# Kernel tuning notes

Measured on AMD Instinct MI355X. Metric: run time of the kernel, lower is better.

Reference implementation:

```python
import jax, jax.numpy as jnp
import numpy as np

IN_EPS = 1e-3   # torch InstanceNorm2d eps in this module
BN_EPS = 1e-5   # torch BatchNorm2d default eps
KNN_K = 6


def instance_norm(x):
    # x: (B, C, N, 1); normalize per (batch, channel) over spatial dims (affine=False)
    m = jnp.mean(x, axis=(2, 3), keepdims=True)
    v = jnp.var(x, axis=(2, 3), keepdims=True)
    return (x - m) / jnp.sqrt(v + IN_EPS)


def batch_norm(x, gamma, beta):
    # training-mode BatchNorm2d: batch statistics over (B, H, W), biased var
    m = jnp.mean(x, axis=(0, 2, 3), keepdims=True)
    v = jnp.var(x, axis=(0, 2, 3), keepdims=True)
    xn = (x - m) / jnp.sqrt(v + BN_EPS)
    return xn * gamma[None, :, None, None] + beta[None, :, None, None]


def conv1x1(x, w, b):
    # x: (B, Cin, N, K), w: (Cout, Cin), b: (Cout,)
    return jnp.einsum('bcnk,oc->bonk', x, w) + b[None, :, None, None]


def graph_feature(x, k):
    # x: (B, C, P). KNN in feature space + edge feature [x_i, x_i - x_j].
    B, C, P = x.shape
    sq = jnp.sum(x * x, axis=1)                      # (B, P)
    gram = jnp.einsum('bcn,bcm->bnm', x, x)          # (B, P, P)
    pd = 2.0 * gram - sq[:, :, None] - sq[:, None, :]  # negative squared distance
    idx = jax.lax.top_k(pd, k)[1]                    # (B, P, k) nearest (incl. self)
    xt = jnp.transpose(x, (0, 2, 1))                 # (B, P, C)
    neigh = jnp.take_along_axis(xt, idx.reshape(B, P * k)[:, :, None], axis=1)
    neigh = neigh.reshape(B, P, k, C)
    center = jnp.broadcast_to(xt[:, :, None, :], (B, P, k, C))
    edge = jnp.concatenate([center, center - neigh], axis=3)  # (B, P, k, 2C)
    return jnp.transpose(edge, (0, 3, 1, 2))         # (B, 2C, P, k)


def reference(data, dp_gamma, dp_beta, dp_w, dp_b, du_gamma, du_beta, du_w, du_b,
              dg_w1, dg_b1, dg_g1, dg_bb1, dg_w2, dg_b2, dg_g2, dg_bb2, sc_w, sc_b):
    x = data                                         # (B, C=128, N, 1)
    # ---- diff_pool ----
    h = jax.nn.relu(batch_norm(instance_norm(x), dp_gamma, dp_beta))
    embed = conv1x1(h, dp_w, dp_b)                   # (B, K=256, N, 1)
    S = jax.nn.softmax(embed[..., 0], axis=2)        # softmax over points -> (B, K, N)
    x_down = jnp.einsum('bcn,bkn->bck', x[..., 0], S)  # (B, C, K)
    feats = jnp.transpose(x_down, (0, 2, 1))         # transpose(1,2): (B, K, C)
    # ---- DGCNN_MAX_Block: channels=K=256, points=C=128, k=6 ----
    edge = graph_feature(feats, KNN_K)               # (B, 2K, C, k)
    g = jax.nn.relu(batch_norm(conv1x1(edge, dg_w1, dg_b1), dg_g1, dg_bb1))
    g = jax.nn.relu(batch_norm(conv1x1(g, dg_w2, dg_b2), dg_g2, dg_bb2))
    g = jnp.max(g, axis=3)                           # max over neighbors -> (B, K, C)
    x2 = jnp.transpose(g, (0, 2, 1))                 # (B, C, K)
    # ---- diff_unpool ----
    h2 = jax.nn.relu(batch_norm(instance_norm(x), du_gamma, du_beta))
    embed2 = conv1x1(h2, du_w, du_b)                 # (B, K, N, 1)
    S2 = jax.nn.softmax(embed2[..., 0], axis=1)      # softmax over clusters -> (B, K, N)
    x_up = jnp.einsum('bck,bkn->bcn', x2, S2)[..., None]  # (B, C, N, 1)
    out = jnp.concatenate([x, x_up], axis=1)         # (B, 2C, N, 1)
    return conv1x1(out, sc_w, sc_b)                  # (B, C, N, 1)


def setup_inputs() -> dict:
    B, C, N, K = 16, 128, 8192, 256
    ks = jax.random.split(jax.random.key(0), 8)
    s = 0.05
    return {
        'data': jax.random.normal(ks[0], (B, C, N, 1), dtype=jnp.float32),
        'dp_gamma': jnp.ones((C,), jnp.float32), 'dp_beta': jnp.zeros((C,), jnp.float32),
        'dp_w': jax.random.normal(ks[1], (K, C), dtype=jnp.float32) * s,
        'dp_b': jnp.zeros((K,), jnp.float32),
        'du_gamma': jnp.ones((C,), jnp.float32), 'du_beta': jnp.zeros((C,), jnp.float32),
        'du_w': jax.random.normal(ks[2], (K, C), dtype=jnp.float32) * s,
        'du_b': jnp.zeros((K,), jnp.float32),
        'dg_w1': jax.random.normal(ks[3], (K, 2 * K), dtype=jnp.float32) * s,
        'dg_b1': jnp.zeros((K,), jnp.float32),
        'dg_g1': jnp.ones((K,), jnp.float32), 'dg_bb1': jnp.zeros((K,), jnp.float32),
        'dg_w2': jax.random.normal(ks[4], (K, K), dtype=jnp.float32) * s,
        'dg_b2': jnp.zeros((K,), jnp.float32),
        'dg_g2': jnp.ones((K,), jnp.float32), 'dg_bb2': jnp.zeros((K,), jnp.float32),
        'sc_w': jax.random.normal(ks[5], (C, 2 * C), dtype=jnp.float32) * s,
        'sc_b': jnp.zeros((C,), jnp.float32),
    }
```

## Files before the change

### kernel.cpp

```cpp
#include <hip/hip_runtime.h>

typedef __attribute__((ext_vector_type(4))) float f32x4;
typedef __attribute__((ext_vector_type(8))) short s16x8;
typedef __attribute__((ext_vector_type(8))) unsigned short u16x8;
typedef __attribute__((ext_vector_type(4))) unsigned short u16x4;

namespace {
constexpr int B_ = 16, C_ = 128, N_ = 8192, K_ = 256, P_ = 128, NB_ = 6;
constexpr int NSP = 16;
}

__device__ __forceinline__ float bf2f(unsigned short h) {
  return __uint_as_float(((unsigned int)h) << 16);
}
__device__ __forceinline__ unsigned short f2bf(float f) {
  unsigned int u = __float_as_uint(f);
  return (unsigned short)((u + 0x7fffu + ((u >> 16) & 1u)) >> 16);
}
__device__ __forceinline__ void gload_lds16(const void* gsrc, void* ldsdst) {
  __builtin_amdgcn_global_load_lds(
      (const __attribute__((address_space(1))) void*)gsrc,
      (__attribute__((address_space(3))) void*)ldsdst, 16, 0, 0);
}

__global__ __launch_bounds__(256) void k_prep(const float* __restrict__ x,
                                              unsigned short* __restrict__ xh,
                                              unsigned short* __restrict__ xcn,
                                              float* __restrict__ pstS,
                                              float* __restrict__ pstQ) {
  const int chunk = blockIdx.x, b = blockIdx.y;
  const int n0 = chunk * 64;
  __shared__ float ts[64][132];
  __shared__ float rs_[2][128], rq_[2][128];
  const int tid = threadIdx.x;
  for (int i = 0; i < 8; i++) {
    int q = tid + i * 256;
    int n4 = q & 15, c = q >> 4;
    float4 v = *reinterpret_cast<const float4*>(x + (size_t)(b * C_ + c) * N_ + n0 + 4 * n4);
    ts[4 * n4 + 0][c] = v.x; ts[4 * n4 + 1][c] = v.y;
    ts[4 * n4 + 2][c] = v.z; ts[4 * n4 + 3][c] = v.w;
    u16x4 p; p[0] = f2bf(v.x); p[1] = f2bf(v.y); p[2] = f2bf(v.z); p[3] = f2bf(v.w);
    *reinterpret_cast<u16x4*>(xcn + (size_t)(b * C_ + c) * N_ + n0 + 4 * n4) = p;
  }
  __syncthreads();
  for (int i = 0; i < 4; i++) {
    int q = tid + i * 256;
    int cg = q & 15, nn = q >> 4;
    u16x8 o;
#pragma unroll
    for (int j = 0; j < 8; j++) o[j] = f2bf(ts[nn][8 * cg + j]);
    *reinterpret_cast<u16x8*>(xh + (size_t)(b * N_ + n0 + nn) * C_ + 8 * cg) = o;
  }
  {
    int c = tid & 127, h = tid >> 7;
    float s = 0.f, ss = 0.f;
    for (int nn = h * 32; nn < h * 32 + 32; nn++) { float v = ts[nn][c]; s += v; ss += v * v; }
    rs_[h][c] = s; rq_[h][c] = ss;
  }
  __syncthreads();
  if (tid < 128) {
    pstS[(chunk * 16 + b) * 128 + tid] = rs_[0][tid] + rs_[1][tid];
    pstQ[(chunk * 16 + b) * 128 + tid] = rq_[0][tid] + rq_[1][tid];
  }
}

__global__ __launch_bounds__(256) void k_wconv(const float* __restrict__ dpw,
                                               const float* __restrict__ duw,
                                               const float* __restrict__ scw,
                                               const float* __restrict__ w1,
                                               const float* __restrict__ w2,
                                               unsigned short* __restrict__ dpwh,
                                               unsigned short* __restrict__ duwh,
                                               unsigned short* __restrict__ scah,
                                               unsigned short* __restrict__ scbh,
                                               unsigned short* __restrict__ w1sh,
                                               unsigned short* __restrict__ w1bh,
                                               unsigned short* __restrict__ w2h) {
  int t = blockIdx.x * 256 + threadIdx.x;
  if (t < 65536) {
    int o = t >> 8, k = t & 255;
    float vb = w1[(size_t)o * 512 + 256 + k];
    w1sh[t] = f2bf(w1[(size_t)o * 512 + k] + vb);
    w1bh[t] = f2bf(vb);
    w2h[t] = f2bf(w2[t]);
  }
  if (t < 32768) { dpwh[t] = f2bf(dpw[t]); duwh[t] = f2bf(duw[t]); }
  if (t < 16384) {
    int o = t >> 7, c = t & 127;
    scah[t] = f2bf(scw[o * 256 + c]);
    scbh[t] = f2bf(scw[o * 256 + 128 + c]);
  }
}

__global__ __launch_bounds__(256) void k_instat_fin(const float* __restrict__ pstS,
                                                    const float* __restrict__ pstQ,
                                                    float* __restrict__ m_o,
                                                    float* __restrict__ v_o,
                                                    float* __restrict__ r_o) {
  int e = blockIdx.x * 256 + threadIdx.x;
  int b = e >> 7, c = e & 127;
  float s = 0.f, q = 0.f;
  for (int ch = 0; ch < 128; ch++) {
    s += pstS[(ch * 16 + b) * 128 + c];
    q += pstQ[(ch * 16 + b) * 128 + c];
  }
  float m = s / N_;
  float v = q / N_ - m * m;
  m_o[e] = m; v_o[e] = v; r_o[e] = rsqrtf(v + 1e-3f);
}

__global__ void k_affine(const float* __restrict__ m_in, const float* __restrict__ v_in,
                         const float* __restrict__ r_in,
                         const float* __restrict__ dpg, const float* __restrict__ dpb,
                         const float* __restrict__ dug, const float* __restrict__ dub,
                         float* __restrict__ a_dp, float* __restrict__ d_dp,
                         float* __restrict__ a_du, float* __restrict__ d_du) {
  int c = threadIdx.x;
  float V = 0.f;
  for (int b = 0; b < B_; b++) { float v = v_in[b * C_ + c]; V += v / (v + 1e-3f); }
  V *= (1.f / B_);
  float R = rsqrtf(V + 1e-5f);
  float gdp = dpg[c], bdp = dpb[c], gdu = dug[c], bdu = dub[c];
  for (int b = 0; b < B_; b++) {
    int i = b * C_ + c;
    float r = r_in[i], m = m_in[i];
    float sdp = r * R * gdp;
    a_dp[i] = sdp; d_dp[i] = -m * sdp + bdp;
    float sdu = r * R * gdu;
    a_du[i] = sdu; d_du[i] = -m * sdu + bdu;
  }
}

__global__ __launch_bounds__(512) void k_dp_fused(const unsigned short* __restrict__ xh,
                                                  const unsigned short* __restrict__ xcn,
                                                  const unsigned short* __restrict__ dpwh,
                                                  const float* __restrict__ a_dp,
                                                  const float* __restrict__ d_dp,
                                                  const float* __restrict__ dpbias,
                                                  float* __restrict__ part,
                                                  float* __restrict__ pS) {
  const int sp = blockIdx.x, b = blockIdx.y;
  const int nbase = sp * (N_ / NSP);
  __shared__ __align__(16) unsigned short bufW[256 * 128];
  __shared__ __align__(16) unsigned short bufH[64 * 128];
  __shared__ __align__(16) unsigned short bufP[256 * 64];
  __shared__ __align__(16) unsigned short bufC[128 * 64];
  __shared__ float bias_s[256], aff_as[128], aff_ds[128];
  const int tid = threadIdx.x, lane = tid & 63, wid = tid >> 6;
  const int wr = wid >> 1, wc = wid & 1, l15 = lane & 15, l4 = lane >> 4;
  if (tid < 256) bias_s[tid] = dpbias[tid];
  if (tid < 128) { aff_as[tid] = a_dp[b * C_ + tid]; aff_ds[tid] = d_dp[b * C_ + tid]; }
#pragma unroll
  for (int i = 0; i < 8; i++) {
    int call = wid * 8 + i;
    int row = call * 4 + (lane >> 4);
    int gch = (lane & 15) ^ (row & 7);
    gload_lds16(dpwh + (size_t)row * C_ + gch * 8, bufW + call * 512);
  }
#pragma unroll
  for (int i = 0; i < 2; i++) {
    int call = wid * 2 + i;
    int row = call * 4 + (lane >> 4);
    int gch = (lane & 15) ^ (row & 7);
    gload_lds16(xh + (size_t)(b * N_ + nbase + row) * C_ + gch * 8, bufH + call * 512);
  }
#pragma unroll
  for (int i = 0; i < 2; i++) {
    int call = wid * 2 + i;
    int row = call * 8 + (lane >> 3);
    int gch = (lane & 7) ^ (row & 7);
    gload_lds16(xcn + (size_t)(b * C_ + row) * N_ + nbase + gch * 8, bufC + call * 512);
  }
  __syncthreads();
#pragma unroll
  for (int i = 0; i < 2; i++) {
    int q = tid + i * 512;
    int row = q >> 4, p = q & 15;
    int cb = (p ^ (row & 7)) * 8;
    u16x8 v = *reinterpret_cast<const u16x8*>(bufH + q * 8);
    u16x8 h;
#pragma unroll
    for (int j = 0; j < 8; j++)
      h[j] = f2bf(fmaxf(fmaf(aff_as[cb + j], bf2f(v[j]), aff_ds[cb + j]), 0.f));
    *reinterpret_cast<u16x8*>(bufH + q * 8) = h;
  }
  __syncthreads();
  s16x8 onesf;
#pragma unroll
  for (int j = 0; j < 8; j++) onesf[j] = (short)0x3F80;
  f32x4 acc2[2][8] = {};
  f32x4 accS[8] = {};
  for (int nc = 0; nc < N_ / NSP; nc += 64) {
    const int n0n = nbase + nc + 64;
    const bool more = (nc + 64) < (N_ / NSP);
    f32x4 acc1[4][2] = {};
#pragma unroll
    for (int ks = 0; ks < 128; ks += 32) {
      const int ch = (ks >> 3) + l4;
      s16x8 af[4], bh[2];
#pragma unroll
      for (int m = 0; m < 4; m++) {
        int row = wr * 64 + m * 16 + l15;
        af[m] = *reinterpret_cast<const s16x8*>(bufW + row * 128 + ((ch ^ (row & 7)) << 3));
      }
#pragma unroll
      for (int nq = 0; nq < 2; nq++) {
        int row = wc * 32 + nq * 16 + l15;
        bh[nq] = *reinterpret_cast<const s16x8*>(bufH + row * 128 + ((ch ^ (row & 7)) << 3));
      }
#pragma unroll
      for (int m = 0; m < 4; m++)
#pragma unroll
        for (int nq = 0; nq < 2; nq++)
          acc1[m][nq] = __builtin_amdgcn_mfma_f32_16x16x32_bf16(af[m], bh[nq], acc1[m][nq], 0, 0, 0);
    }
#pragma unroll
    for (int m = 0; m < 4; m++)
#pragma unroll
      for (int nq = 0; nq < 2; nq++) {
        int kl = wr * 64 + m * 16 + 4 * l4;
        int nl = wc * 32 + nq * 16 + l15;
#pragma unroll
        for (int r = 0; r < 4; r++) {
          unsigned short v = f2bf(__expf(acc1[m][nq][r] + bias_s[kl + r]));
          bufP[(kl + r) * 64 + ((((nl >> 3) ^ ((kl + r) & 7)) << 3) | (nl & 7))] = v;
        }
      }
    __syncthreads();
    if (more) {
#pragma unroll
      for (int i = 0; i < 2; i++) {
        int call = wid * 2 + i;
        int row = call * 4 + (lane >> 4);
        int gch = (lane & 15) ^ (row & 7);
        gload_lds16(xh + (size_t)(b * N_ + n0n + row) * C_ + gch * 8, bufH + call * 512);
      }
    }
#pragma unroll
    for (int ks = 0; ks < 64; ks += 32) {
      const int ch = (ks >> 3) + l4;
      s16x8 af2[2], bp[8];
#pragma unroll
      for (int m = 0; m < 2; m++) {
        int row = wr * 32 + m * 16 + l15;
        af2[m] = *reinterpret_cast<const s16x8*>(bufC + row * 64 + ((ch ^ (row & 7)) << 3));
      }
#pragma unroll
      for (int nn = 0; nn < 8; nn++) {
        int row = wc * 128 + nn * 16 + l15;
        bp[nn] = *reinterpret_cast<const s16x8*>(bufP + row * 64 + ((ch ^ (row & 7)) << 3));
      }
#pragma unroll
      for (int m = 0; m < 2; m++)
#pragma unroll
        for (int nn = 0; nn < 8; nn++)
          acc2[m][nn] = __builtin_amdgcn_mfma_f32_16x16x32_bf16(af2[m], bp[nn], acc2[m][nn], 0, 0, 0);
      if (wr == 0) {
#pragma unroll
        for (int nn = 0; nn < 8; nn++)
          accS[nn] = __builtin_amdgcn_mfma_f32_16x16x32_bf16(onesf, bp[nn], accS[nn], 0, 0, 0);
      }
    }
    __syncthreads();
    if (more) {
#pragma unroll
      for (int i = 0; i < 2; i++) {
        int q = tid + i * 512;
        int row = q >> 4, p = q & 15;
        int cb = (p ^ (row & 7)) * 8;
        u16x8 v = *reinterpret_cast<const u16x8*>(bufH + q * 8);
        u16x8 h;
#pragma unroll
        for (int j = 0; j < 8; j++)
          h[j] = f2bf(fmaxf(fmaf(aff_as[cb + j], bf2f(v[j]), aff_ds[cb + j]), 0.f));
        *reinterpret_cast<u16x8*>(bufH + q * 8) = h;
      }
#pragma unroll
      for (int i = 0; i < 2; i++) {
        int call = wid * 2 + i;
        int row = call * 8 + (lane >> 3);
        int gch = (lane & 7) ^ (row & 7);
        gload_lds16(xcn + (size_t)(b * C_ + row) * N_ + n0n + gch * 8, bufC + call * 512);
      }
      __syncthreads();
    }
  }
#pragma unroll
  for (int m = 0; m < 2; m++)
#pragma unroll
    for (int nn = 0; nn < 8; nn++) {
      int c = wr * 32 + m * 16 + 4 * l4;
      int k = wc * 128 + nn * 16 + l15;
#pragma unroll
      for (int r = 0; r < 4; r++)
        part[((size_t)(sp * B_ + b) * C_ + c + r) * K_ + k] = acc2[m][nn][r];
    }
  if (wr == 0 && l4 == 0) {
#pragma unroll
    for (int nn = 0; nn < 8; nn++)
      pS[((size_t)sp * 16 + b) * 256 + wc * 128 + nn * 16 + l15] = accS[nn][0];
  }
}

__global__ __launch_bounds__(256) void k_rowfin(const float* __restrict__ pS,
                                                float* __restrict__ rden) {
  int e = blockIdx.x * 256 + threadIdx.x;
  int b = e >> 8, k = e & 255;
  float s = 0.f;
  for (int sp = 0; sp < NSP; sp++) s += pS[((size_t)sp * 16 + b) * 256 + k];
  rden[e] = 1.f / s;
}

__global__ __launch_bounds__(256) void k_xdown_red(const float* __restrict__ part,
                                                   const float* __restrict__ rden,
                                                   float* __restrict__ xd,
                                                   unsigned short* __restrict__ xdh) {
  int e = blockIdx.x * 256 + threadIdx.x;
  int k = e % K_;
  int b = e / (K_ * C_);
  float s = 0.f;
  for (int sp = 0; sp < NSP; sp++) s += part[(size_t)sp * (B_ * C_ * K_) + e];
  float v = s * rden[b * K_ + k];
  xd[e] = v;
  xdh[e] = f2bf(v);
}

__global__ __launch_bounds__(256) void k_knn(const float* __restrict__ xd,
                                             int* __restrict__ idx) {
  const int p0 = blockIdx.x * 8, b = blockIdx.y;
  __shared__ float A[8][256];
  __shared__ float Bt[32][132];
  __shared__ float pd_s[8][129];
  __shared__ float sq_s[128], sqh[128];
  const int tid = threadIdx.x;
#pragma unroll
  for (int i = 0; i < 2; i++) {
    int t = tid + i * 256;
    int pp = t >> 6, k4 = t & 63;
    float4 v = *reinterpret_cast<const float4*>(xd + (size_t)(b * C_ + p0 + pp) * K_ + 4 * k4);
    *reinterpret_cast<float4*>(&A[pp][4 * k4]) = v;
  }
  const int q = tid & 127, h = tid >> 7;
  float acc[4] = {};
  float sqacc = 0.f;
  for (int k0 = 0; k0 < K_; k0 += 32) {
    for (int i = 0; i < 4; i++) {
      int t = tid + i * 256;
      int qq = t >> 3, k4 = t & 7;
      float4 v = *reinterpret_cast<const float4*>(xd + (size_t)(b * C_ + qq) * K_ + k0 + 4 * k4);
      Bt[4 * k4 + 0][qq] = v.x; Bt[4 * k4 + 1][qq] = v.y;
      Bt[4 * k4 + 2][qq] = v.z; Bt[4 * k4 + 3][qq] = v.w;
    }
    __syncthreads();
    for (int kk = 0; kk < 32; ++kk) {
      float bv = Bt[kk][q];
#pragma unroll
      for (int i = 0; i < 4; ++i) acc[i] = fmaf(A[h * 4 + i][k0 + kk], bv, acc[i]);
    }
    {
      float s = 0.f;
      for (int kk = h * 16; kk < h * 16 + 16; kk++) { float v = Bt[kk][q]; s += v * v; }
      sqacc += s;
    }
    __syncthreads();
  }
  if (h == 1) sqh[q] = sqacc;
#pragma unroll
  for (int i = 0; i < 4; ++i) pd_s[h * 4 + i][q] = acc[i];
  __syncthreads();
  if (tid < 128) sq_s[tid] = sqacc + sqh[tid];
  __syncthreads();
  const int wv = tid >> 6, lane = tid & 63;
  for (int r = 0; r < 2; r++) {
    int p = wv * 2 + r;
    float v0 = 2.f * pd_s[p][lane] - sq_s[lane];
    float v1 = 2.f * pd_s[p][lane + 64] - sq_s[lane + 64];
    int q0 = lane, q1 = lane + 64;
#pragma unroll
    for (int j = 0; j < NB_; j++) {
      float bv; int bq;
      if (v0 > v1 || (v0 == v1 && q0 < q1)) { bv = v0; bq = q0; } else { bv = v1; bq = q1; }
#pragma unroll
      for (int o = 32; o > 0; o >>= 1) {
        float ov = __shfl_xor(bv, o); int oq = __shfl_xor(bq, o);
        if (ov > bv || (ov == bv && oq < bq)) { bv = ov; bq = oq; }
      }
      if (lane == 0) idx[(b * P_ + p0 + p) * NB_ + j] = bq;
      if (q0 == bq) v0 = -3.0e38f;
      if (q1 == bq) v1 = -3.0e38f;
    }
  }
}

__global__ __launch_bounds__(256) void k_uv_mfma(const unsigned short* __restrict__ xdh,
                                                 const unsigned short* __restrict__ w1sh,
                                                 const unsigned short* __restrict__ w1bh,
                                                 float* __restrict__ Ut, float* __restrict__ Vt) {
  const int o0 = blockIdx.x * 128, which = blockIdx.y, b = blockIdx.z;
  __shared__ __align__(16) unsigned char smemraw[128 * 132 * 4];
  unsigned short* tA = (unsigned short*)smemraw;
  unsigned short* tB = tA + 128 * 128;
  const unsigned short* wsel = which ? w1bh : w1sh;
  const int tid = threadIdx.x, lane = tid & 63, wid = tid >> 6;
  const int wr = wid >> 1, wc = wid & 1, l15 = lane & 15, l4 = lane >> 4;
  f32x4 acc[4][4] = {};
  for (int kh = 0; kh < 256; kh += 128) {
#pragma unroll
    for (int i = 0; i < 8; i++) {
      int call = wid * 8 + i;
      int row = call * 4 + (lane >> 4);
      int gch = (lane & 15) ^ (row & 7);
      gload_lds16(wsel + (size_t)(o0 + row) * 256 + kh + gch * 8, tA + call * 512);
      gload_lds16(xdh + (size_t)(b * P_ + row) * 256 + kh + gch * 8, tB + call * 512);
    }
    __syncthreads();
#pragma unroll
    for (int ks = 0; ks < 128; ks += 32) {
      const int ch = (ks >> 3) + l4;
      s16x8 af[4], bfv[4];
#pragma unroll
      for (int m = 0; m < 4; m++) {
        int row = wr * 64 + m * 16 + l15;
        af[m] = *reinterpret_cast<const s16x8*>(tA + row * 128 + ((ch ^ (row & 7)) << 3));
      }
#pragma unroll
      for (int n = 0; n < 4; n++) {
        int row = wc * 64 + n * 16 + l15;
        bfv[n] = *reinterpret_cast<const s16x8*>(tB + row * 128 + ((ch ^ (row & 7)) << 3));
      }
#pragma unroll
      for (int m = 0; m < 4; m++)
#pragma unroll
        for (int n = 0; n < 4; n++)
          acc[m][n] = __builtin_amdgcn_mfma_f32_16x16x32_bf16(af[m], bfv[n], acc[m][n], 0, 0, 0);
    }
    __syncthreads();
  }
  float (*ef)[132] = (float(*)[132])smemraw;
#pragma unroll
  for (int m = 0; m < 4; m++)
#pragma unroll
    for (int n = 0; n < 4; n++) {
      int ol = wr * 64 + m * 16 + 4 * l4;
      int pl = wc * 64 + n * 16 + l15;
#pragma unroll
      for (int r = 0; r < 4; r++) ef[pl][ol + r] = acc[m][n][r];
    }
  __syncthreads();
  float* outp = which ? Vt : Ut;
  for (int i = 0; i < 16; i++) {
    int q = tid + i * 256;
    int pl = q >> 5, c4 = q & 31;
    float4 v = *reinterpret_cast<const float4*>(&ef[pl][c4 * 4]);
    *reinterpret_cast<float4*>(outp + (size_t)(b * P_ + pl) * 256 + o0 + c4 * 4) = v;
  }
}

__global__ __launch_bounds__(256) void k_edge_t(const float* __restrict__ Ut,
                                                const float* __restrict__ Vt,
                                                const int* __restrict__ idx,
                                                const float* __restrict__ b1,
                                                unsigned short* __restrict__ g1h) {
  __shared__ float b1s[256];
  const int tid = threadIdx.x;
  b1s[tid] = b1[tid];
  __syncthreads();
  const int row0 = blockIdx.x * 16;
  for (int r = 0; r < 16; r++) {
    int row = row0 + r;
    int b = row / 768, pj = row % 768, p = pj / 6;
    int q = idx[(b * P_ + p) * NB_ + (pj % 6)];
    float v = Ut[(size_t)(b * P_ + p) * 256 + tid] + b1s[tid]
            - Vt[(size_t)(b * P_ + q) * 256 + tid];
    g1h[(size_t)row * 256 + tid] = f2bf(v);
  }
}

__global__ __launch_bounds__(256) void k_bnstat_t(const unsigned short* __restrict__ gt,
                                                  float* __restrict__ partS,
                                                  float* __restrict__ partQ) {
  const int tid = threadIdx.x;
  const size_t row0 = (size_t)blockIdx.x * 256;
  float s = 0.f, ss = 0.f;
  for (int r = 0; r < 256; r++) {
    float v = bf2f(gt[(row0 + r) * 256 + tid]);
    s += v; ss += v * v;
  }
  partS[blockIdx.x * 256 + tid] = s;
  partQ[blockIdx.x * 256 + tid] = ss;
}

__global__ __launch_bounds__(256) void k_conv2_mfma(const unsigned short* __restrict__ g1h,
                                                    const unsigned short* __restrict__ w2h,
                                                    const float* __restrict__ b2,
                                                    const float* __restrict__ partS,
                                                    const float* __restrict__ partQ,
                                                    const float* __restrict__ gamma,
                                                    const float* __restrict__ beta,
                                                    unsigned short* __restrict__ g2h) {
  const int n0 = blockIdx.x * 128, o0 = blockIdx.y * 128, b = blockIdx.z;
  __shared__ __align__(16) unsigned short smem[2 * 128 * 128];
  unsigned short* tA = smem;
  unsigned short* tB = smem + 128 * 128;
  __shared__ float scs[256], shs[256], b2s[128];
  const int tid = threadIdx.x, lane = tid & 63, wid = tid >> 6;
  const int wr = wid >> 1, wc = wid & 1, l15 = lane & 15, l4 = lane >> 4;
  {
    float s = 0.f, q = 0.f;
    for (int i = 0; i < 48; i++) { s += partS[i * 256 + tid]; q += partQ[i * 256 + tid]; }
    const float cnt = (float)(B_ * P_ * NB_);
    float m = s / cnt, var = q / cnt - m * m;
    float scale = gamma[tid] * rsqrtf(var + 1e-5f);
    scs[tid] = scale; shs[tid] = -m * scale + beta[tid];
  }
  if (tid < 128) b2s[tid] = b2[o0 + tid];
  f32x4 acc[4][4] = {};
  for (int kh = 0; kh < 256; kh += 128) {
#pragma unroll
    for (int i = 0; i < 8; i++) {
      int call = wid * 8 + i;
      int row = call * 4 + (lane >> 4);
      int gch = (lane & 15) ^ (row & 7);
      gload_lds16(w2h + (size_t)(o0 + row) * 256 + kh + gch * 8, tA + call * 512);
      gload_lds16(g1h + (size_t)(b * 768 + n0 + row) * 256 + kh + gch * 8, tB + call * 512);
    }
    __syncthreads();
#pragma unroll
    for (int ks = 0; ks < 128; ks += 32) {
      const int ch = (ks >> 3) + l4;
      s16x8 af[4], bfv[4];
#pragma unroll
      for (int m = 0; m < 4; m++) {
        int row = wr * 64 + m * 16 + l15;
        af[m] = *reinterpret_cast<const s16x8*>(tA + row * 128 + ((ch ^ (row & 7)) << 3));
      }
#pragma unroll
      for (int n = 0; n < 4; n++) {
        int row = wc * 64 + n * 16 + l15;
        s16x8 raw = *reinterpret_cast<const s16x8*>(tB + row * 128 + ((ch ^ (row & 7)) << 3));
        s16x8 h;
#pragma unroll
        for (int j = 0; j < 8; j++) {
          int c = kh + ks + 8 * l4 + j;
          h[j] = (short)f2bf(fmaxf(fmaf(scs[c], bf2f((unsigned short)raw[j]), shs[c]), 0.f));
        }
        bfv[n] = h;
      }
#pragma unroll
      for (int m = 0; m < 4; m++)
#pragma unroll
        for (int n = 0; n < 4; n++)
          acc[m][n] = __builtin_amdgcn_mfma_f32_16x16x32_bf16(af[m], bfv[n], acc[m][n], 0, 0, 0);
    }
    __syncthreads();
  }
  unsigned short (*e_s)[136] = reinterpret_cast<unsigned short(*)[136]>(smem);
#pragma unroll
  for (int m = 0; m < 4; m++)
#pragma unroll
    for (int n = 0; n < 4; n++) {
      int ol = wr * 64 + m * 16 + 4 * l4;
      int nl = wc * 64 + n * 16 + l15;
#pragma unroll
      for (int r = 0; r < 4; r++)
        e_s[nl][ol + r] = f2bf(acc[m][n][r] + b2s[ol + r]);
    }
  __syncthreads();
  for (int i = 0; i < 8; i++) {
    int q = tid + i * 256;
    int og = q & 15, nl = q >> 4;
    u16x8 v = *reinterpret_cast<const u16x8*>(&e_s[nl][8 * og]);
    *reinterpret_cast<u16x8*>(g2h + (size_t)(b * 768 + n0 + nl) * 256 + o0 + 8 * og) = v;
  }
}

__global__ __launch_bounds__(256) void k_gmax_t(const unsigned short* __restrict__ g2h,
                                                const float* __restrict__ partS,
                                                const float* __restrict__ partQ,
                                                const float* __restrict__ gamma,
                                                const float* __restrict__ beta,
                                                unsigned short* __restrict__ gmaxh) {
  const int o0 = blockIdx.x * 128, b = blockIdx.y;
  __shared__ float scS[128], shS[128];
  const int tid = threadIdx.x;
  if (tid < 128) {
    int o = o0 + tid;
    float s = 0.f, q = 0.f;
    for (int i = 0; i < 48; i++) { s += partS[i * 256 + o]; q += partQ[i * 256 + o]; }
    const float cnt = (float)(B_ * P_ * NB_);
    float m = s / cnt, var = q / cnt - m * m;
    float scale = gamma[o] * rsqrtf(var + 1e-5f);
    scS[tid] = scale; shS[tid] = -m * scale + beta[o];
  }
  __syncthreads();
  const int ol = tid & 127, ph = tid >> 7;
  const int o = o0 + ol;
  const float sc = scS[ol], sh = shS[ol];
  for (int p8 = ph * 64; p8 < ph * 64 + 64; p8 += 8) {
    u16x8 pack;
#pragma unroll
    for (int pi = 0; pi < 8; pi++) {
      int p = p8 + pi;
      float m = 0.f;
#pragma unroll
      for (int j = 0; j < NB_; j++) {
        float v = bf2f(g2h[(size_t)(b * 768 + p * 6 + j) * 256 + o]);
        m = fmaxf(m, fmaf(sc, v, sh));
      }
      pack[pi] = f2bf(m);
    }
    *reinterpret_cast<u16x8*>(gmaxh + (size_t)(b * 256 + o) * P_ + p8) = pack;
  }
}

__global__ __launch_bounds__(256) void k_m2_mfma(const unsigned short* __restrict__ gmaxh,
                                                 const unsigned short* __restrict__ scbh,
                                                 unsigned short* __restrict__ M2h) {
  const int k0 = blockIdx.x * 128, b = blockIdx.y;
  __shared__ __align__(16) unsigned short smem[2 * 128 * 128];
  unsigned short* tA = smem;
  unsigned short* tB = smem + 128 * 128;
  const int tid = threadIdx.x, lane = tid & 63, wid = tid >> 6;
  const int wr = wid >> 1, wc = wid & 1, l15 = lane & 15, l4 = lane >> 4;
#pragma unroll
  for (int i = 0; i < 8; i++) {
    int call = wid * 8 + i;
    int row = call * 4 + (lane >> 4);
    int gch = (lane & 15) ^ (row & 7);
    gload_lds16(scbh + (size_t)row * P_ + gch * 8, tA + call * 512);
    gload_lds16(gmaxh + (size_t)(b * 256 + k0 + row) * P_ + gch * 8, tB + call * 512);
  }
  __syncthreads();
  f32x4 acc[4][4] = {};
#pragma unroll
  for (int ks = 0; ks < 128; ks += 32) {
    const int ch = (ks >> 3) + l4;
    s16x8 af[4], bfv[4];
#pragma unroll
    for (int m = 0; m < 4; m++) {
      int row = wr * 64 + m * 16 + l15;
      af[m] = *reinterpret_cast<const s16x8*>(tA + row * 128 + ((ch ^ (row & 7)) << 3));
    }
#pragma unroll
    for (int n = 0; n < 4; n++) {
      int row = wc * 64 + n * 16 + l15;
      bfv[n] = *reinterpret_cast<const s16x8*>(tB + row * 128 + ((ch ^ (row & 7)) << 3));
    }
#pragma unroll
    for (int m = 0; m < 4; m++)
#pragma unroll
      for (int n = 0; n < 4; n++)
        acc[m][n] = __builtin_amdgcn_mfma_f32_16x16x32_bf16(af[m], bfv[n], acc[m][n], 0, 0, 0);
  }
  __syncthreads();
  unsigned short (*e_s)[136] = reinterpret_cast<unsigned short(*)[136]>(smem);
#pragma unroll
  for (int m = 0; m < 4; m++)
#pragma unroll
    for (int n = 0; n < 4; n++) {
      int ol = wr * 64 + m * 16 + 4 * l4;
      int kl = wc * 64 + n * 16 + l15;
#pragma unroll
      for (int r = 0; r < 4; r++)
        e_s[ol + r][kl] = f2bf(acc[m][n][r]);
    }
  __syncthreads();
  for (int i = 0; i < 8; i++) {
    int q = tid + i * 256;
    int kg = q & 15, oo = q >> 4;
    u16x8 v = *reinterpret_cast<const u16x8*>(&e_s[oo][8 * kg]);
    *reinterpret_cast<u16x8*>(M2h + (size_t)(b * C_ + oo) * K_ + k0 + 8 * kg) = v;
  }
}

__global__ __launch_bounds__(512) void k_final_f(const unsigned short* __restrict__ xh,
                                                 const unsigned short* __restrict__ duwh,
                                                 const float* __restrict__ dubias,
                                                 const float* __restrict__ a_du,
                                                 const float* __restrict__ d_du,
                                                 const unsigned short* __restrict__ M2h,
                                                 const unsigned short* __restrict__ scah,
                                                 const float* __restrict__ scb,
                                                 float* __restrict__ out) {
  const int n0 = blockIdx.x * 64, b = blockIdx.y;
  __shared__ __align__(16) unsigned short bufX[64 * 128];
  __shared__ __align__(16) unsigned short bufA[128 * 128];
  __shared__ __align__(16) unsigned short bufP[64 * 128];
  __shared__ float aff_as[128], aff_ds[128], scb_s[128], bias_s[128];
  __shared__ float psum_s[64], psum2[4][64];
  const int tid = threadIdx.x, lane = tid & 63, wid = tid >> 6;
  const int wr = wid >> 1, wc = wid & 1, l15 = lane & 15, l4 = lane >> 4;
  if (tid < 128) {
    aff_as[tid] = a_du[b * C_ + tid];
    aff_ds[tid] = d_du[b * C_ + tid];
    scb_s[tid] = scb[tid];
  }
  if (tid < 64) psum_s[tid] = 0.f;
#pragma unroll
  for (int i = 0; i < 2; i++) {
    int call = wid * 2 + i;
    int row = call * 4 + (lane >> 4);
    int gch = (lane & 15) ^ (row & 7);
    gload_lds16(xh + (size_t)(b * N_ + n0 + row) * C_ + gch * 8, bufX + call * 512);
  }
#pragma unroll
  for (int i = 0; i < 4; i++) {
    int call = wid * 4 + i;
    int row = call * 4 + (lane >> 4);
    int gch = (lane & 15) ^ (row & 7);
    gload_lds16(scah + (size_t)row * C_ + gch * 8, bufA + call * 512);
  }
  __syncthreads();
  f32x4 accA[2][2] = {};
#pragma unroll
  for (int ks = 0; ks < 128; ks += 32) {
    const int ch = (ks >> 3) + l4;
    s16x8 af[2], bh[2];
#pragma unroll
    for (int m = 0; m < 2; m++) {
      int row = wr * 32 + m * 16 + l15;
      af[m] = *reinterpret_cast<const s16x8*>(bufA + row * 128 + ((ch ^ (row & 7)) << 3));
    }
#pragma unroll
    for (int nq = 0; nq < 2; nq++) {
      int row = wc * 32 + nq * 16 + l15;
      bh[nq] = *reinterpret_cast<const s16x8*>(bufX + row * 128 + ((ch ^ (row & 7)) << 3));
    }
#pragma unroll
    for (int m = 0; m < 2; m++)
#pragma unroll
      for (int nq = 0; nq < 2; nq++)
        accA[m][nq] = __builtin_amdgcn_mfma_f32_16x16x32_bf16(af[m], bh[nq], accA[m][nq], 0, 0, 0);
  }
  __syncthreads();
#pragma unroll
  for (int i = 0; i < 2; i++) {
    int q = tid + i * 512;
    int row = q >> 4, p = q & 15;
    int cb = (p ^ (row & 7)) * 8;
    u16x8 v = *reinterpret_cast<const u16x8*>(bufX + q * 8);
    u16x8 h;
#pragma unroll
    for (int j = 0; j < 8; j++)
      h[j] = f2bf(fmaxf(fmaf(aff_as[cb + j], bf2f(v[j]), aff_ds[cb + j]), 0.f));
    *reinterpret_cast<u16x8*>(bufX + q * 8) = h;
  }
  f32x4 acc[2][2] = {};
  for (int kh = 0; kh < K_; kh += 128) {
    if (tid < 128) bias_s[tid] = dubias[kh + tid];
#pragma unroll
    for (int i = 0; i < 4; i++) {
      int call = wid * 4 + i;
      int row = call * 4 + (lane >> 4);
      int gch = (lane & 15) ^ (row & 7);
      gload_lds16(duwh + (size_t)(kh + row) * C_ + gch * 8, bufA + call * 512);
    }
    __syncthreads();
    f32x4 acc1[2][2] = {};
#pragma unroll
    for (int ks = 0; ks < 128; ks += 32) {
      const int ch = (ks >> 3) + l4;
      s16x8 af[2], bh[2];
#pragma unroll
      for (int m = 0; m < 2; m++) {
        int row = wr * 32 + m * 16 + l15;
        af[m] = *reinterpret_cast<const s16x8*>(bufA + row * 128 + ((ch ^ (row & 7)) << 3));
      }
#pragma unroll
      for (int nq = 0; nq < 2; nq++) {
        int row = wc * 32 + nq * 16 + l15;
        bh[nq] = *reinterpret_cast<const s16x8*>(bufX + row * 128 + ((ch ^ (row & 7)) << 3));
      }
#pragma unroll
      for (int m = 0; m < 2; m++)
#pragma unroll
        for (int nq = 0; nq < 2; nq++)
          acc1[m][nq] = __builtin_amdgcn_mfma_f32_16x16x32_bf16(af[m], bh[nq], acc1[m][nq], 0, 0, 0);
    }
    __syncthreads();
#pragma unroll
    for (int i = 0; i < 4; i++) {
      int call = wid * 4 + i;
      int row = call * 4 + (lane >> 4);
      int gch = (lane & 15) ^ (row & 7);
      gload_lds16(M2h + (size_t)(b * C_ + row) * K_ + kh + gch * 8, bufA + call * 512);
    }
    float pn[2] = {0.f, 0.f};
#pragma unroll
    for (int m = 0; m < 2; m++)
#pragma unroll
      for (int nq = 0; nq < 2; nq++) {
        int kl = wr * 32 + m * 16 + 4 * l4;
        int nl = wc * 32 + nq * 16 + l15;
        u16x4 pk;
#pragma unroll
        for (int r = 0; r < 4; r++) {
          unsigned short v = f2bf(__expf(acc1[m][nq][r] + bias_s[kl + r]));
          pk[r] = v;
          pn[nq] += bf2f(v);
        }
        int swzbase = (((kl >> 3) ^ (nl & 7)) << 3) | (kl & 7);
        *reinterpret_cast<u16x4*>(bufP + nl * 128 + swzbase) = pk;
      }
#pragma unroll
    for (int nq = 0; nq < 2; nq++) {
      pn[nq] += __shfl_xor(pn[nq], 16);
      pn[nq] += __shfl_xor(pn[nq], 32);
      if (l4 == 0) psum2[wr][wc * 32 + nq * 16 + l15] = pn[nq];
    }
    __syncthreads();
    if (tid < 64)
      psum_s[tid] += psum2[0][tid] + psum2[1][tid] + psum2[2][tid] + psum2[3][tid];
#pragma unroll
    for (int ks = 0; ks < 128; ks += 32) {
      const int ch = (ks >> 3) + l4;
      s16x8 af[2], bh[2];
#pragma unroll
      for (int m = 0; m < 2; m++) {
        int row = wr * 32 + m * 16 + l15;
        af[m] = *reinterpret_cast<const s16x8*>(bufA + row * 128 + ((ch ^ (row & 7)) << 3));
      }
#pragma unroll
      for (int nq = 0; nq < 2; nq++) {
        int row = wc * 32 + nq * 16 + l15;
        bh[nq] = *reinterpret_cast<const s16x8*>(bufP + row * 128 + ((ch ^ (row & 7)) << 3));
      }
#pragma unroll
      for (int m = 0; m < 2; m++)
#pragma unroll
        for (int nq = 0; nq < 2; nq++)
          acc[m][nq] = __builtin_amdgcn_mfma_f32_16x16x32_bf16(af[m], bh[nq], acc[m][nq], 0, 0, 0);
    }
    __syncthreads();
  }
#pragma unroll
  for (int m = 0; m < 2; m++)
#pragma unroll
    for (int nq = 0; nq < 2; nq++) {
      float rv = 1.f / psum_s[wc * 32 + nq * 16 + l15];
      int o = wr * 32 + m * 16 + 4 * l4;
      int nn = n0 + wc * 32 + nq * 16 + l15;
#pragma unroll
      for (int r = 0; r < 4; r++)
        out[(size_t)(b * C_ + o + r) * N_ + nn] =
            acc[m][nq][r] * rv + accA[m][nq][r] + scb_s[o + r];
    }
}

extern "C" void kernel_launch(void* const* d_in, const int* in_sizes, int n_in,
                              void* d_out, int out_size, void* d_ws, size_t ws_size,
                              hipStream_t stream) {
  (void)in_sizes; (void)n_in; (void)out_size; (void)ws_size;
  const float* x      = (const float*)d_in[0];
  const float* dpg    = (const float*)d_in[1];
  const float* dpb    = (const float*)d_in[2];
  const float* dpw    = (const float*)d_in[3];
  const float* dpbias = (const float*)d_in[4];
  const float* dug    = (const float*)d_in[5];
  const float* dub    = (const float*)d_in[6];
  const float* duw    = (const float*)d_in[7];
  const float* dubias = (const float*)d_in[8];
  const float* w1     = (const float*)d_in[9];
  const float* b1     = (const float*)d_in[10];
  const float* g1g    = (const float*)d_in[11];
  const float* g1b    = (const float*)d_in[12];
  const float* w2     = (const float*)d_in[13];
  const float* b2     = (const float*)d_in[14];
  const float* g2g    = (const float*)d_in[15];
  const float* g2b    = (const float*)d_in[16];
  const float* scw    = (const float*)d_in[17];
  const float* scb    = (const float*)d_in[18];
  float* out = (float*)d_out;
  float* ws  = (float*)d_ws;

  float* part = ws;
  unsigned short* g1h   = (unsigned short*)ws;
  unsigned short* g2h   = g1h + 3145728;
  unsigned short* gmaxh = g2h + 3145728;
  unsigned short* xh  = (unsigned short*)(ws + 16777216);
  unsigned short* xcn = (unsigned short*)(ws + 25165824);
  float* base  = ws + 33554432;
  float* m_in  = base;
  float* v_in  = m_in + 2048;
  float* r_in  = v_in + 2048;
  float* a_dp  = r_in + 2048;
  float* d_dp  = a_dp + 2048;
  float* a_du  = d_dp + 2048;
  float* d_du  = a_du + 2048;
  float* rden  = d_du + 2048;
  float* xd    = rden + 4096;
  float* Ut    = xd + 524288;
  float* Vt    = Ut + 524288;
  int*   idxb  = (int*)(Vt + 524288);
  float* partS = (float*)(idxb + 12288);
  float* partQ = partS + 12288;
  float* pstS  = partQ + 12288;
  float* pstQ  = pstS + 262144;
  float* pS    = pstQ + 262144;
  unsigned short* xdh  = (unsigned short*)(pS + 65536);
  unsigned short* dpwh = xdh + 524288;
  unsigned short* duwh = dpwh + 32768;
  unsigned short* scah = duwh + 32768;
  unsigned short* scbh = scah + 16384;
  unsigned short* w1sh = scbh + 16384;
  unsigned short* w1bh = w1sh + 65536;
  unsigned short* w2h  = w1bh + 65536;
  unsigned short* M2h  = w2h + 65536;

  k_prep<<<dim3(128, 16), 256, 0, stream>>>(x, xh, xcn, pstS, pstQ);
  k_wconv<<<dim3(256), 256, 0, stream>>>(dpw, duw, scw, w1, w2,
                                         dpwh, duwh, scah, scbh, w1sh, w1bh, w2h);
  k_instat_fin<<<dim3(8), 256, 0, stream>>>(pstS, pstQ, m_in, v_in, r_in);
  k_affine<<<1, 128, 0, stream>>>(m_in, v_in, r_in, dpg, dpb, dug, dub, a_dp, d_dp, a_du, d_du);
  k_dp_fused<<<dim3(NSP, 16), 512, 0, stream>>>(xh, xcn, dpwh, a_dp, d_dp, dpbias, part, pS);
  k_rowfin<<<dim3(16), 256, 0, stream>>>(pS, rden);
  k_xdown_red<<<dim3(2048), 256, 0, stream>>>(part, rden, xd, xdh);
  k_knn<<<dim3(16, 16), 256, 0, stream>>>(xd, idxb);
  k_uv_mfma<<<dim3(2, 2, 16), 256, 0, stream>>>(xdh, w1sh, w1bh, Ut, Vt);
  k_edge_t<<<dim3(768), 256, 0, stream>>>(Ut, Vt, idxb, b1, g1h);
  k_bnstat_t<<<dim3(48), 256, 0, stream>>>(g1h, partS, partQ);
  k_conv2_mfma<<<dim3(6, 2, 16), 256, 0, stream>>>(g1h, w2h, b2, partS, partQ, g1g, g1b, g2h);
  k_bnstat_t<<<dim3(48), 256, 0, stream>>>(g2h, partS, partQ);
  k_gmax_t<<<dim3(2, 16), 256, 0, stream>>>(g2h, partS, partQ, g2g, g2b, gmaxh);
  k_m2_mfma<<<dim3(2, 16), 256, 0, stream>>>(gmaxh, scbh, M2h);
  k_final_f<<<dim3(128, 16), 512, 0, stream>>>(xh, duwh, dubias, a_du, d_du, M2h, scah, scb, out);
}
```

Baseline: 208.3 us.

## Derive channel-major x tile in LDS instead of writing and reloading xcn

Stops k_prep from writing a second channel-major bf16 copy of the input (xcn) and stops k_dp_fused from loading it. The fused kernel now loads the point-major xh tile into a new raw buffer and transposes it into bufC with scalar LDS stores while applying the affine+ReLU. This removes a full global write and read of the bf16 input, at the cost of an extra LDS buffer (more shared memory per block) and many scattered 2-byte LDS writes that may cause bank conflicts.

After: 214.4 us. 2.9% more time.

```diff
diff --git a/kernel.cpp b/kernel.cpp
--- a/kernel.cpp
+++ b/kernel.cpp
@@ -25,7 +25,6 @@
 
 __global__ __launch_bounds__(256) void k_prep(const float* __restrict__ x,
                                               unsigned short* __restrict__ xh,
-                                              unsigned short* __restrict__ xcn,
                                               float* __restrict__ pstS,
                                               float* __restrict__ pstQ) {
   const int chunk = blockIdx.x, b = blockIdx.y;
@@ -39,8 +38,6 @@
     float4 v = *reinterpret_cast<const float4*>(x + (size_t)(b * C_ + c) * N_ + n0 + 4 * n4);
     ts[4 * n4 + 0][c] = v.x; ts[4 * n4 + 1][c] = v.y;
     ts[4 * n4 + 2][c] = v.z; ts[4 * n4 + 3][c] = v.w;
-    u16x4 p; p[0] = f2bf(v.x); p[1] = f2bf(v.y); p[2] = f2bf(v.z); p[3] = f2bf(v.w);
-    *reinterpret_cast<u16x4*>(xcn + (size_t)(b * C_ + c) * N_ + n0 + 4 * n4) = p;
   }
   __syncthreads();
   for (int i = 0; i < 4; i++) {
@@ -132,7 +129,6 @@
 }
 
 __global__ __launch_bounds__(512) void k_dp_fused(const unsigned short* __restrict__ xh,
-                                                  const unsigned short* __restrict__ xcn,
                                                   const unsigned short* __restrict__ dpwh,
                                                   const float* __restrict__ a_dp,
                                                   const float* __restrict__ d_dp,
@@ -142,6 +138,7 @@
   const int sp = blockIdx.x, b = blockIdx.y;
   const int nbase = sp * (N_ / NSP);
   __shared__ __align__(16) unsigned short bufW[256 * 128];
+  __shared__ __align__(16) unsigned short bufR[64 * 128];
   __shared__ __align__(16) unsigned short bufH[64 * 128];
   __shared__ __align__(16) unsigned short bufP[256 * 64];
   __shared__ __align__(16) unsigned short bufC[128 * 64];
@@ -162,14 +159,7 @@
     int call = wid * 2 + i;
     int row = call * 4 + (lane >> 4);
     int gch = (lane & 15) ^ (row & 7);
-    gload_lds16(xh + (size_t)(b * N_ + nbase + row) * C_ + gch * 8, bufH + call * 512);
-  }
-#pragma unroll
-  for (int i = 0; i < 2; i++) {
-    int call = wid * 2 + i;
-    int row = call * 8 + (lane >> 3);
-    int gch = (lane & 7) ^ (row & 7);
-    gload_lds16(xcn + (size_t)(b * C_ + row) * N_ + nbase + gch * 8, bufC + call * 512);
+    gload_lds16(xh + (size_t)(b * N_ + nbase + row) * C_ + gch * 8, bufR + call * 512);
   }
   __syncthreads();
 #pragma unroll
@@ -177,11 +167,14 @@
     int q = tid + i * 512;
     int row = q >> 4, p = q & 15;
     int cb = (p ^ (row & 7)) * 8;
-    u16x8 v = *reinterpret_cast<const u16x8*>(bufH + q * 8);
+    u16x8 v = *reinterpret_cast<const u16x8*>(bufR + q * 8);
     u16x8 h;
 #pragma unroll
-    for (int j = 0; j < 8; j++)
+    for (int j = 0; j < 8; j++) {
       h[j] = f2bf(fmaxf(fmaf(aff_as[cb + j], bf2f(v[j]), aff_ds[cb + j]), 0.f));
+      int c = cb + j;
+      bufC[c * 64 + ((((row >> 3) ^ (c & 7)) << 3) | (row & 7))] = v[j];
+    }
     *reinterpret_cast<u16x8*>(bufH + q * 8) = h;
   }
   __syncthreads();
@@ -233,7 +226,7 @@
         int call = wid * 2 + i;
         int row = call * 4 + (lane >> 4);
         int gch = (lane & 15) ^ (row & 7);
-        gload_lds16(xh + (size_t)(b * N_ + n0n + row) * C_ + gch * 8, bufH + call * 512);
+        gload_lds16(xh + (size_t)(b * N_ + n0n + row) * C_ + gch * 8, bufR + call * 512);
       }
     }
 #pragma unroll
@@ -268,19 +261,15 @@
         int q = tid + i * 512;
         int row = q >> 4, p = q & 15;
         int cb = (p ^ (row & 7)) * 8;
-        u16x8 v = *reinterpret_cast<const u16x8*>(bufH + q * 8);
+        u16x8 v = *reinterpret_cast<const u16x8*>(bufR + q * 8);
         u16x8 h;
 #pragma unroll
-        for (int j = 0; j < 8; j++)
+        for (int j = 0; j < 8; j++) {
           h[j] = f2bf(fmaxf(fmaf(aff_as[cb + j], bf2f(v[j]), aff_ds[cb + j]), 0.f));
+          int c = cb + j;
+          bufC[c * 64 + ((((row >> 3) ^ (c & 7)) << 3) | (row & 7))] = v[j];
+        }
         *reinterpret_cast<u16x8*>(bufH + q * 8) = h;
-      }
-#pragma unroll
-      for (int i = 0; i < 2; i++) {
-        int call = wid * 2 + i;
-        int row = call * 8 + (lane >> 3);
-        int gch = (lane & 7) ^ (row & 7);
-        gload_lds16(xcn + (size_t)(b * C_ + row) * N_ + n0n + gch * 8, bufC + call * 512);
       }
       __syncthreads();
     }
@@ -878,7 +867,6 @@
   unsigned short* g2h   = g1h + 3145728;
   unsigned short* gmaxh = g2h + 3145728;
   unsigned short* xh  = (unsigned short*)(ws + 16777216);
-  unsigned short* xcn = (unsigned short*)(ws + 25165824);
   float* base  = ws + 33554432;
   float* m_in  = base;
   float* v_in  = m_in + 2048;
@@ -907,12 +895,12 @@
   unsigned short* w2h  = w1bh + 65536;
   unsigned short* M2h  = w2h + 65536;
 
-  k_prep<<<dim3(128, 16), 256, 0, stream>>>(x, xh, xcn, pstS, pstQ);
+  k_prep<<<dim3(128, 16), 256, 0, stream>>>(x, xh, pstS, pstQ);
   k_wconv<<<dim3(256), 256, 0, stream>>>(dpw, duw, scw, w1, w2,
                                          dpwh, duwh, scah, scbh, w1sh, w1bh, w2h);
   k_instat_fin<<<dim3(8), 256, 0, stream>>>(pstS, pstQ, m_in, v_in, r_in);
   k_affine<<<1, 128, 0, stream>>>(m_in, v_in, r_in, dpg, dpb, dug, dub, a_dp, d_dp, a_du, d_du);
-  k_dp_fused<<<dim3(NSP, 16), 512, 0, stream>>>(xh, xcn, dpwh, a_dp, d_dp, dpbias, part, pS);
+  k_dp_fused<<<dim3(NSP, 16), 512, 0, stream>>>(xh, dpwh, a_dp, d_dp, dpbias, part, pS);
   k_rowfin<<<dim3(16), 256, 0, stream>>>(pS, rden);
   k_xdown_red<<<dim3(2048), 256, 0, stream>>>(part, rden, xd, xdh);
   k_knn<<<dim3(16, 16), 256, 0, stream>>>(xd, idxb);
```
